# Performance work log

Hardware: AMD Instinct MI355X
Metric: run time of the kernel (lower is better)

Reference implementation:

```python
import jax, jax.numpy as jnp
import numpy as np

EPS_NORM = 1e-12  # F.normalize eps
LN_EPS = 1e-5


def _ln(x, g, b):
    mu = x.mean(-1, keepdims=True)
    var = ((x - mu) ** 2).mean(-1, keepdims=True)
    return (x - mu) / jnp.sqrt(var + LN_EPS) * g + b


def _gate(x, w1, b1, g, b, w2, b2):
    # Linear -> LayerNorm(32) -> SiLU -> Linear -> Sigmoid, squeeze(-1)
    t = _ln(x @ w1 + b1, g, b)
    t = jax.nn.silu(t)
    return jax.nn.sigmoid(t @ w2 + b2)[..., 0]


def setup_inputs() -> dict:
    key = jax.random.key(0)
    B, N, D, dH, S, HID = 4, 4096, 1024, 256, 256, 32
    ks = jax.random.split(key, 24)
    sc_d = 0.5 * (6.0 / (D + dH)) ** 0.5  # xavier gain=0.5 approx
    sc_h = 0.5 * (6.0 / (D + HID)) ** 0.5
    inp = {
        "h": jax.random.normal(ks[0], (B, N, D), jnp.float32),
        # encoder complex projection (stored as (in,out))
        "Wr": jax.random.uniform(ks[1], (D, dH), jnp.float32, -sc_d, sc_d),
        "br": jnp.zeros((dH,), jnp.float32),
        "Wi": jax.random.uniform(ks[2], (D, dH), jnp.float32, -sc_d, sc_d),
        "bi": jnp.zeros((dH,), jnp.float32),
        # uncertainty net
        "uw1": jax.random.uniform(ks[3], (D, HID), jnp.float32, -sc_h, sc_h),
        "ub1": jnp.zeros((HID,), jnp.float32),
        "ug": jnp.ones((HID,), jnp.float32),
        "ubeta": jnp.zeros((HID,), jnp.float32),
        "uw2": jax.random.uniform(ks[4], (HID, 1), jnp.float32, -0.2, 0.2),
        "ub2": jnp.zeros((1,), jnp.float32),
        # decoherence gamma net
        "gw1": jax.random.uniform(ks[5], (D, HID), jnp.float32, -sc_h, sc_h),
        "gb1": jnp.zeros((HID,), jnp.float32),
        "gg": jnp.ones((HID,), jnp.float32),
        "gbeta": jnp.zeros((HID,), jnp.float32),
        "gw2": jax.random.uniform(ks[6], (HID, 1), jnp.float32, -0.2, 0.2),
        "gb2": jnp.zeros((1,), jnp.float32),
        # memory attention params
        "m_real": jax.random.normal(ks[7], (S, dH), jnp.float32) / dH ** 0.5,
        "m_imag": jax.random.normal(ks[8], (S, dH), jnp.float32) / dH ** 0.5,
        "values": jax.random.normal(ks[9], (S, D), jnp.float32) * 0.02,
        "ow": jax.random.uniform(ks[10], (D, D), jnp.float32, -0.5 * (3.0 / D) ** 0.5, 0.5 * (3.0 / D) ** 0.5),
        "ob": jnp.zeros((D,), jnp.float32),
        # norms
        "n1g": jnp.ones((D,), jnp.float32),
        "n1b": jnp.zeros((D,), jnp.float32),
        "n2g": jnp.ones((D,), jnp.float32),
        "n2b": jnp.zeros((D,), jnp.float32),
        # FFN
        "fw1": jax.random.normal(ks[11], (D, 4 * D), jnp.float32) * (2.0 / (5 * D)) ** 0.5,
        "fb1": jnp.zeros((4 * D,), jnp.float32),
        "fw2": jax.random.normal(ks[12], (4 * D, D), jnp.float32) * (2.0 / (5 * D)) ** 0.5,
        "fb2": jnp.zeros((D,), jnp.float32),
    }
    return inp


def reference(h, Wr, br, Wi, bi,
              uw1, ub1, ug, ubeta, uw2, ub2,
              gw1, gb1, gg, gbeta, gw2, gb2,
              m_real, m_imag, values, ow, ob,
              n1g, n1b, n2g, n2b, fw1, fb1, fw2, fb2):
    dH = m_real.shape[-1]
    # --- QuantumStateEncoder: psi = normalize(complex(Wr h, Wi h)), p in [0,0.95]
    pr = h @ Wr + br                       # (B,N,dH) real part
    pi = h @ Wi + bi                       # (B,N,dH) imag part
    nrm = jnp.maximum(jnp.sqrt(jnp.sum(pr * pr + pi * pi, -1, keepdims=True)), EPS_NORM)
    pr, pi = pr / nrm, pi / nrm
    p_init = _gate(h, uw1, ub1, ug, ubeta, uw2, ub2) * 0.95   # (B,N)
    # --- ContextualDecoherenceLayer: ctx = mean over N (identical per token)
    ctx = h.mean(axis=1)                   # (B,D)
    gamma = _gate(ctx, gw1, gb1, gg, gbeta, gw2, gb2)          # (B,)
    p = p_init * (1.0 - gamma[:, None])    # (B,N)
    # --- ExternalQuantumMemoryAttention
    mnrm = jnp.maximum(jnp.sqrt(jnp.sum(m_real * m_real + m_imag * m_imag, -1, keepdims=True)), EPS_NORM)
    Mr, Mi = m_real / mnrm, m_imag / mnrm  # (S,dH)
    # <psi|m> = sum conj(psi)*m ; |.|^2 is re^2+im^2
    re = jnp.einsum('bnd,sd->bns', pr, Mr) + jnp.einsum('bnd,sd->bns', pi, Mi)
    im = jnp.einsum('bnd,sd->bns', pr, Mi) - jnp.einsum('bnd,sd->bns', pi, Mr)
    overlap = re * re + im * im            # (B,N,S)
    raw = (1.0 - p)[..., None] * overlap + (p / dH)[..., None]
    attn = raw / (raw.sum(-1, keepdims=True) + 1e-8)
    attn_out = jnp.einsum('bns,sd->bnd', attn, values) @ ow + ob
    # --- residual + LN + FFN (dropout = eval identity)
    h1 = _ln(h + attn_out, n1g, n1b)
    ff = jax.nn.gelu(h1 @ fw1 + fb1, approximate=False) @ fw2 + fb2
    return _ln(h1 + ff, n2g, n2b)
```

## Files before the change

kernel.cpp:

```cpp
#include <hip/hip_runtime.h>
#include <math.h>


#define B_ 4
#define N_ 4096
#define D_ 1024
#define DH_ 256
#define S_ 256
#define HID_ 32
#define M_ (B_ * N_)

typedef unsigned short u16;
typedef unsigned int u32;
typedef __attribute__((ext_vector_type(8))) short bfrag;
typedef __attribute__((ext_vector_type(4))) float ffrag;

__device__ __forceinline__ float b2f(u16 u) {
    return __uint_as_float(((unsigned)u) << 16);
}
__device__ __forceinline__ u16 f2b(float f) {
    unsigned u = __float_as_uint(f);
    return (u16)((u + 0x7FFFu + ((u >> 16) & 1u)) >> 16);
}
__device__ __forceinline__ float fast_erf(float x) {
    float ax = fabsf(x);
    float t = __builtin_amdgcn_rcpf(fmaf(0.3275911f, ax, 1.f));
    float p = t * fmaf(t, fmaf(t, fmaf(t, fmaf(t, 1.061405429f, -1.453152027f),
                                       1.421413741f), -0.284496736f),
                       0.254829592f);
    float e = __expf(-ax * ax);
    float y = fmaf(-p, e, 1.f);
    return copysignf(y, x);
}
__device__ __forceinline__ float gelu_fast(float x) {
    return 0.5f * x * (1.0f + fast_erf(x * 0.70710678118654752440f));
}
__device__ __forceinline__ float ldf(const void* p, size_t i, bool bf) {
    return bf ? b2f(((const u16*)p)[i]) : ((const float*)p)[i];
}
__device__ __forceinline__ bool detect_bf(const void* n1g) {
    return *(const unsigned*)n1g == 0x3F803F80u;
}
__device__ __forceinline__ void gload16(const void* g, void* lds) {
    __builtin_amdgcn_global_load_lds(
        (const __attribute__((address_space(1))) u32*)g,
        (__attribute__((address_space(3))) u32*)lds, 16, 0, 0);
}

__global__ void zero_kernel(float* __restrict__ p, int n) {
    int i = blockIdx.x * 256 + threadIdx.x;
    if (i < n) p[i] = 0.f;
}

__global__ __launch_bounds__(256)
void h2b_kernel(const void* __restrict__ h, u16* __restrict__ hB,
                const void* __restrict__ n1g) {
    const bool bf = detect_bf(n1g);
    const size_t i = ((size_t)blockIdx.x * 256 + threadIdx.x) * 8;
    if (bf) {
        *(uint4*)(hB + i) = *(const uint4*)((const u16*)h + i);
    } else {
        const float* hf = (const float*)h;
        float4 x = *(const float4*)(hf + i);
        float4 y = *(const float4*)(hf + i + 4);
        union { u16 u[8]; uint4 v; } pk;
        pk.u[0] = f2b(x.x); pk.u[1] = f2b(x.y);
        pk.u[2] = f2b(x.z); pk.u[3] = f2b(x.w);
        pk.u[4] = f2b(y.x); pk.u[5] = f2b(y.y);
        pk.u[6] = f2b(y.z); pk.u[7] = f2b(y.w);
        *(uint4*)(hB + i) = pk.v;
    }
}

__global__ void pack_bias_kernel(const void* __restrict__ br,
                                 const void* __restrict__ bi,
                                 void* __restrict__ brbi,
                                 const void* __restrict__ n1g) {
    const bool bf = detect_bf(n1g);
    const int t = threadIdx.x;
    if (bf) {
        ((u16*)brbi)[t]       = ((const u16*)br)[t];
        ((u16*)brbi)[256 + t] = ((const u16*)bi)[t];
    } else {
        ((float*)brbi)[t]       = ((const float*)br)[t];
        ((float*)brbi)[256 + t] = ((const float*)bi)[t];
    }
}

__global__ __launch_bounds__(256)
void transpose_w_kernel(const void* __restrict__ W, u16* __restrict__ WT,
                        int K, int N, const void* __restrict__ n1g) {
    const bool bf = detect_bf(n1g);
    __shared__ u16 t[64][65];
    const int n0 = blockIdx.x * 64, k0 = blockIdx.y * 64;
    const int a = threadIdx.x & 63, b = threadIdx.x >> 6;
#pragma unroll
    for (int r = 0; r < 16; ++r) {
        int k = b * 16 + r;
        t[k][a] = f2b(ldf(W, (size_t)(k0 + k) * N + n0 + a, bf));
    }
    __syncthreads();
#pragma unroll
    for (int r = 0; r < 16; ++r) {
        int n = b * 16 + r;
        WT[(size_t)(n0 + n) * K + k0 + a] = t[a][n];
    }
}

__global__ __launch_bounds__(256)
void ctx_sum_kernel(const u16* __restrict__ hB, float* __restrict__ ctx) {
    const int chunks = N_ / 128;
    const int b = blockIdx.x / chunks;
    const int ch = blockIdx.x % chunks;
    const int tid = threadIdx.x;
    const int colg = (tid & 127) * 8;
    const int rp = tid >> 7;
    const size_t base = ((size_t)b * N_ + (size_t)ch * 128) * D_;
    float a[8] = {};
    for (int r = rp; r < 128; r += 2) {
        uint4 v = *(const uint4*)(hB + base + (size_t)r * D_ + colg);
        const u16* u = (const u16*)&v;
#pragma unroll
        for (int q = 0; q < 8; ++q) a[q] += b2f(u[q]);
    }
#pragma unroll
    for (int q = 0; q < 8; ++q)
        atomicAdd(&ctx[b * D_ + colg + q], a[q]);
}

__global__ __launch_bounds__(128)
void gamma_gate_kernel(const float* __restrict__ ctx,
                       const void* __restrict__ w1, const void* __restrict__ b1,
                       const void* __restrict__ g, const void* __restrict__ beta,
                       const void* __restrict__ w2, const void* __restrict__ b2,
                       float* __restrict__ out, const void* __restrict__ n1g) {
    const bool bf = detect_bf(n1g);
    const int row = blockIdx.x;
    const int tid = threadIdx.x;
    const int col = tid & 31;
    const int chunk = tid >> 5;
    const float xscale = 1.f / (float)N_;

    float acc = 0.f;
    for (int k = chunk * 256; k < chunk * 256 + 256; ++k)
        acc += ctx[(size_t)row * D_ + k] * xscale * ldf(w1, (size_t)k * HID_ + col, bf);

    __shared__ float part[4][HID_];
    __shared__ float s[HID_];
    __shared__ float mu_s, rstd_s;
    part[chunk][col] = acc;
    __syncthreads();
    if (tid < HID_)
        s[tid] = part[0][tid] + part[1][tid] + part[2][tid] + part[3][tid]
               + ldf(b1, tid, bf);
    __syncthreads();
    if (tid == 0) {
        float m = 0.f;
        for (int i = 0; i < HID_; ++i) m += s[i];
        m /= (float)HID_;
        float var = 0.f;
        for (int i = 0; i < HID_; ++i) { float dd = s[i] - m; var += dd * dd; }
        var /= (float)HID_;
        mu_s = m;
        rstd_s = rsqrtf(var + 1e-5f);
    }
    __syncthreads();
    if (tid < HID_) {
        float v = (s[tid] - mu_s) * rstd_s * ldf(g, tid, bf) + ldf(beta, tid, bf);
        v = v / (1.f + expf(-v));
        s[tid] = v * ldf(w2, tid, bf);
    }
    __syncthreads();
    if (tid == 0) {
        float z = 0.f;
        for (int i = 0; i < HID_; ++i) z += s[i];
        z += ldf(b2, 0, bf);
        out[row] = 1.f / (1.f + expf(-z));
    }
}

__global__ __launch_bounds__(128)
void p_gate_kernel(const u16* __restrict__ hB,
                   const void* __restrict__ w1, const void* __restrict__ b1,
                   const void* __restrict__ g, const void* __restrict__ beta,
                   const void* __restrict__ w2, const void* __restrict__ b2,
                   float* __restrict__ out, const void* __restrict__ n1g) {
    const bool bf = detect_bf(n1g);
    const int row = blockIdx.x;
    const int tid = threadIdx.x;
    const int col = tid & 31;
    const int chunk = tid >> 5;

    float acc = 0.f;
    for (int k = chunk * 256; k < chunk * 256 + 256; ++k)
        acc += b2f(hB[(size_t)row * D_ + k]) * ldf(w1, (size_t)k * HID_ + col, bf);

    __shared__ float part[4][HID_];
    __shared__ float s[HID_];
    __shared__ float mu_s, rstd_s;
    part[chunk][col] = acc;
    __syncthreads();
    if (tid < HID_)
        s[tid] = part[0][tid] + part[1][tid] + part[2][tid] + part[3][tid]
               + ldf(b1, tid, bf);
    __syncthreads();
    if (tid == 0) {
        float m = 0.f;
        for (int i = 0; i < HID_; ++i) m += s[i];
        m /= (float)HID_;
        float var = 0.f;
        for (int i = 0; i < HID_; ++i) { float dd = s[i] - m; var += dd * dd; }
        var /= (float)HID_;
        mu_s = m;
        rstd_s = rsqrtf(var + 1e-5f);
    }
    __syncthreads();
    if (tid < HID_) {
        float v = (s[tid] - mu_s) * rstd_s * ldf(g, tid, bf) + ldf(beta, tid, bf);
        v = v / (1.f + expf(-v));
        s[tid] = v * ldf(w2, tid, bf);
    }
    __syncthreads();
    if (tid == 0) {
        float z = 0.f;
        for (int i = 0; i < HID_; ++i) z += s[i];
        z += ldf(b2, 0, bf);
        out[row] = 0.95f / (1.f + expf(-z));
    }
}

__global__ __launch_bounds__(256)
void norm_m_kernel(const void* __restrict__ m_real, const void* __restrict__ m_imag,
                   u16* __restrict__ bcatT, const void* __restrict__ n1g) {
    const bool bf = detect_bf(n1g);
    const int s = blockIdx.x;
    const int d = threadIdx.x;
    float mr = ldf(m_real, (size_t)s * DH_ + d, bf);
    float mi = ldf(m_imag, (size_t)s * DH_ + d, bf);
    float v = mr * mr + mi * mi;
#pragma unroll
    for (int off = 32; off; off >>= 1) v += __shfl_down(v, off, 64);
    __shared__ float red[4];
    if ((d & 63) == 0) red[d >> 6] = v;
    __syncthreads();
    float tot = red[0] + red[1] + red[2] + red[3];
    float inv = 1.f / fmaxf(sqrtf(tot), 1e-12f);
    float nr = mr * inv, ni = mi * inv;
    bcatT[(size_t)s * 512 + d]               = f2b(nr);
    bcatT[(size_t)s * 512 + 256 + d]         = f2b(ni);
    bcatT[(size_t)(256 + s) * 512 + d]       = f2b(ni);
    bcatT[(size_t)(256 + s) * 512 + 256 + d] = f2b(-nr);
}

__global__ __launch_bounds__(256)
void gemm_mfma(const u16* __restrict__ A, const u16* __restrict__ WT,
               const void* __restrict__ bias, void* __restrict__ out,
               int kseg, int lda, int ldw, int ldo,
               int act, int fo32, const void* __restrict__ n1g) {
    const bool bf = detect_bf(n1g);
    __shared__ short As[128 * 64];
    __shared__ short Bs[128 * 64];
    const int tid = threadIdx.x;

    const int nwg = gridDim.x * gridDim.y;
    const int flat = blockIdx.y * gridDim.x + blockIdx.x;
    const int xcd = flat & 7, idx = flat >> 3;
    const int qq = nwg >> 3, rr = nwg & 7;
    const int nf = (xcd < rr ? xcd * (qq + 1) : rr * (qq + 1) + (xcd - rr) * qq) + idx;
    const int c0 = (nf % gridDim.x) * 128;
    const int r0 = (nf / gridDim.x) * 128;

    const int lane = tid & 63, wave = tid >> 6;
    const int wm = wave & 1, wn = wave >> 1;
    const int quad = lane >> 4, l15 = lane & 15;
    const int l8 = lane >> 3;
    const int lc = (lane & 7) ^ l8;
    const int sx = l15 & 7;

    ffrag acc[4][4];
#pragma unroll
    for (int i = 0; i < 4; ++i)
#pragma unroll
        for (int j = 0; j < 4; ++j)
            acc[i][j] = (ffrag){0.f, 0.f, 0.f, 0.f};

    for (int k0 = 0; k0 < kseg; k0 += 64) {
        __syncthreads();
#pragma unroll
        for (int i = 0; i < 4; ++i) {
            int rb = wave * 32 + i * 8;
            gload16(A + (size_t)(r0 + rb + l8) * lda + k0 + lc * 8, &As[rb * 64]);
        }
#pragma unroll
        for (int i = 0; i < 4; ++i) {
            int rb = wave * 32 + i * 8;
            gload16(WT + (size_t)(c0 + rb + l8) * ldw + k0 + lc * 8, &Bs[rb * 64]);
        }
        __syncthreads();

#pragma unroll
        for (int ks = 0; ks < 2; ++ks) {
            bfrag a[4], b[4];
#pragma unroll
            for (int i = 0; i < 4; ++i) {
                int row = wm * 64 + i * 16 + l15;
                a[i] = *(const bfrag*)&As[row * 64 + (((ks * 4 + quad) ^ sx) * 8)];
            }
#pragma unroll
            for (int j = 0; j < 4; ++j) {
                int row = wn * 64 + j * 16 + l15;
                b[j] = *(const bfrag*)&Bs[row * 64 + (((ks * 4 + quad) ^ sx) * 8)];
            }
#pragma unroll
            for (int i = 0; i < 4; ++i)
#pragma unroll
                for (int j = 0; j < 4; ++j)
                    acc[i][j] = __builtin_amdgcn_mfma_f32_16x16x32_bf16(
                        a[i], b[j], acc[i][j], 0, 0, 0);
        }
    }

    float bv[4];
#pragma unroll
    for (int j = 0; j < 4; ++j)
        bv[j] = bias ? ldf(bias, c0 + wn * 64 + j * 16 + l15, bf) : 0.f;
#pragma unroll
    for (int i = 0; i < 4; ++i)
#pragma unroll
        for (int r = 0; r < 4; ++r) {
            int row_g = r0 + wm * 64 + i * 16 + quad * 4 + r;
#pragma unroll
            for (int j = 0; j < 4; ++j) {
                int col_g = c0 + wn * 64 + j * 16 + l15;
                float v = acc[i][j][r] + bv[j];
                if (act) v = gelu_fast(v);
                if (fo32) ((float*)out)[(size_t)row_g * ldo + col_g] = v;
                else      ((u16*)out)[(size_t)row_g * ldo + col_g] = f2b(v);
            }
        }
}

__global__ __launch_bounds__(512, 2)
void gemm_mfma2(const u16* __restrict__ A, const u16* __restrict__ WT,
                const void* __restrict__ bias, void* __restrict__ out,
                int K, int lda, int ldw, int ldo,
                int act, int fo32, const void* __restrict__ n1g) {
    const bool bf = detect_bf(n1g);
    __shared__ short As[2][256 * 64];
    __shared__ short Bs[2][256 * 64];
    const int tid = threadIdx.x;

    const int nwg = gridDim.x * gridDim.y;
    const int flat = blockIdx.y * gridDim.x + blockIdx.x;
    const int xcd = flat & 7, idx = flat >> 3;
    const int qq = nwg >> 3, rr = nwg & 7;
    const int nf = (xcd < rr ? xcd * (qq + 1) : rr * (qq + 1) + (xcd - rr) * qq) + idx;
    const int c0 = (nf % gridDim.x) * 256;
    const int r0 = (nf / gridDim.x) * 256;

    const int lane = tid & 63, wave = tid >> 6;
    const int wm = wave & 1, wn = wave >> 1;
    const int quad = lane >> 4, l15 = lane & 15;
    const int l8 = lane >> 3;
    const int lc = (lane & 7) ^ l8;
    const int sx = l15 & 7;

    ffrag acc[8][4];
#pragma unroll
    for (int i = 0; i < 8; ++i)
#pragma unroll
        for (int j = 0; j < 4; ++j)
            acc[i][j] = (ffrag){0.f, 0.f, 0.f, 0.f};

    auto STAGE_PIECE = [&](int buf, int k0, int pc) {
        int rb = pc * 64 + wave * 8;
        gload16(A + (size_t)(r0 + rb + l8) * lda + k0 + lc * 8,
                &As[buf][rb * 64]);
        gload16(WT + (size_t)(c0 + rb + l8) * ldw + k0 + lc * 8,
                &Bs[buf][rb * 64]);
    };

    bfrag a[8], b[4];
    auto PHASE_DS = [&](int buf, int ks) {
#pragma unroll
        for (int j = 0; j < 4; ++j) {
            int row = wn * 64 + j * 16 + l15;
            b[j] = *(const bfrag*)&Bs[buf][row * 64 + (((ks * 4 + quad) ^ sx) * 8)];
        }
#pragma unroll
        for (int i = 0; i < 8; ++i) {
            int row = wm * 128 + i * 16 + l15;
            a[i] = *(const bfrag*)&As[buf][row * 64 + (((ks * 4 + quad) ^ sx) * 8)];
        }
    };
    auto PHASE_MFMA = [&]() {
#pragma unroll
        for (int i = 0; i < 8; ++i)
#pragma unroll
            for (int j = 0; j < 4; ++j)
                acc[i][j] = __builtin_amdgcn_mfma_f32_16x16x32_bf16(
                    a[i], b[j], acc[i][j], 0, 0, 0);
    };

    const int nt = K >> 6;
#pragma unroll
    for (int pc = 0; pc < 4; ++pc) STAGE_PIECE(0, 0, pc);
    int cur = 0;
    for (int t = 0; t < nt; ++t) {
        const int kn = (t + 1) << 6;
        const bool pre = (t + 1 < nt);
        if (pre) {
            STAGE_PIECE(cur ^ 1, kn, 0);
            STAGE_PIECE(cur ^ 1, kn, 1);
            asm volatile("s_waitcnt vmcnt(4)" ::: "memory");
        } else {
            asm volatile("s_waitcnt vmcnt(0)" ::: "memory");
        }
        __builtin_amdgcn_s_barrier();
        PHASE_DS(cur, 0);
        asm volatile("s_waitcnt lgkmcnt(0)" ::: "memory");
        __builtin_amdgcn_sched_barrier(0);
        __builtin_amdgcn_s_setprio(1);
        PHASE_MFMA();
        __builtin_amdgcn_s_setprio(0);
        __builtin_amdgcn_sched_barrier(0);
        PHASE_DS(cur, 1);
        if (pre) {
            STAGE_PIECE(cur ^ 1, kn, 2);
            STAGE_PIECE(cur ^ 1, kn, 3);
        }
        __builtin_amdgcn_s_barrier();
        asm volatile("s_waitcnt lgkmcnt(0)" ::: "memory");
        __builtin_amdgcn_sched_barrier(0);
        __builtin_amdgcn_s_setprio(1);
        PHASE_MFMA();
        __builtin_amdgcn_s_setprio(0);
        __builtin_amdgcn_sched_barrier(0);
        __builtin_amdgcn_s_barrier();
        cur ^= 1;
    }

    float bv[4];
#pragma unroll
    for (int j = 0; j < 4; ++j)
        bv[j] = bias ? ldf(bias, c0 + wn * 64 + j * 16 + l15, bf) : 0.f;
#pragma unroll
    for (int i = 0; i < 8; ++i)
#pragma unroll
        for (int r = 0; r < 4; ++r) {
            int row_g = r0 + wm * 128 + i * 16 + quad * 4 + r;
#pragma unroll
            for (int j = 0; j < 4; ++j) {
                int col_g = c0 + wn * 64 + j * 16 + l15;
                float v = acc[i][j][r] + bv[j];
                if (act) v = gelu_fast(v);
                if (fo32) ((float*)out)[(size_t)row_g * ldo + col_g] = v;
                else      ((u16*)out)[(size_t)row_g * ldo + col_g] = f2b(v);
            }
        }
}

#define TPW 8
__global__ __launch_bounds__(256)
void attn_weights_kernel(const u16* __restrict__ psi,
                         const float* __restrict__ reim,
                         const float* __restrict__ p_init,
                         const float* __restrict__ gamma,
                         u16* __restrict__ a2) {
    const int token0 = blockIdx.x * TPW;
    const int tid = threadIdx.x;
    __shared__ float red[4];

    for (int tt = 0; tt < TPW; ++tt) {
        const size_t t = (size_t)(token0 + tt);
        float x0 = b2f(psi[t * 512 + tid]);
        float x1 = b2f(psi[t * 512 + 256 + tid]);
        float v = x0 * x0 + x1 * x1;
#pragma unroll
        for (int off = 32; off; off >>= 1) v += __shfl_down(v, off, 64);
        if ((tid & 63) == 0) red[tid >> 6] = v;
        __syncthreads();
        float inv = 1.f / fmaxf(red[0] + red[1] + red[2] + red[3], 1e-24f);

        float p = p_init[t] * (1.f - gamma[t / N_]);
        float re = reim[t * 512 + tid];
        float im = reim[t * 512 + 256 + tid];
        float raw = (1.f - p) * (re * re + im * im) * inv + p * (1.f / (float)DH_);

        float w = raw;
#pragma unroll
        for (int off = 32; off; off >>= 1) w += __shfl_down(w, off, 64);
        __syncthreads();
        if ((tid & 63) == 0) red[tid >> 6] = w;
        __syncthreads();
        float denom = red[0] + red[1] + red[2] + red[3];
        a2[t * 256 + tid] = f2b(raw / (denom + 1e-8f));
        __syncthreads();
    }
}

__global__ __launch_bounds__(256)
void copy_rows_kernel(const u16* __restrict__ src, u16* __restrict__ dst) {
    const int row = blockIdx.x;
    const int tid = threadIdx.x;
#pragma unroll
    for (int q = 0; q < 4; ++q)
        dst[(size_t)row * D_ + q * 256 + tid] = src[(size_t)row * D_ + q * 256 + tid];
}

__global__ __launch_bounds__(256)
void ln_add_kernel(const void* __restrict__ x, int xmode, size_t xrow0,
                   const void* __restrict__ y, int ymode,
                   const void* __restrict__ g, const void* __restrict__ b,
                   u16* __restrict__ outB, float* __restrict__ outF,
                   const void* __restrict__ n1g) {
    const bool bfin = detect_bf(n1g);
    const bool bfx = (xmode == 1) ? true : bfin;
    const int row = blockIdx.x;
    const int tid = threadIdx.x;
    __shared__ float red[4];

    float v[4];
#pragma unroll
    for (int q = 0; q < 4; ++q) {
        int d = q * 256 + tid;
        float yv = ymode ? ((const float*)y)[(size_t)row * D_ + d]
                         : b2f(((const u16*)y)[(size_t)row * D_ + d]);
        v[q] = ldf(x, (xrow0 + row) * (size_t)D_ + d, bfx) + yv;
    }

    float s = v[0] + v[1] + v[2] + v[3];
#pragma unroll
    for (int off = 32; off; off >>= 1) s += __shfl_down(s, off, 64);
    if ((tid & 63) == 0) red[tid >> 6] = s;
    __syncthreads();
    float mu = (red[0] + red[1] + red[2] + red[3]) * (1.f / (float)D_);
    __syncthreads();

    float q2 = 0.f;
#pragma unroll
    for (int j = 0; j < 4; ++j) { float dd = v[j] - mu; q2 += dd * dd; }
#pragma unroll
    for (int off = 32; off; off >>= 1) q2 += __shfl_down(q2, off, 64);
    if ((tid & 63) == 0) red[tid >> 6] = q2;
    __syncthreads();
    float var = (red[0] + red[1] + red[2] + red[3]) * (1.f / (float)D_);
    float rstd = rsqrtf(var + 1e-5f);

#pragma unroll
    for (int q = 0; q < 4; ++q) {
        int d = q * 256 + tid;
        float o = (v[q] - mu) * rstd * ldf(g, d, bfin) + ldf(b, d, bfin);
        if (outF) outF[(size_t)row * D_ + d] = o;
        else      outB[(size_t)row * D_ + d] = f2b(o);
    }
}

extern "C" void kernel_launch(void* const* d_in, const int* in_sizes, int n_in,
                              void* d_out, int out_size, void* d_ws, size_t ws_size,
                              hipStream_t stream) {
    const void* h      = d_in[0];
    const void* Wr     = d_in[1];
    const void* br     = d_in[2];
    const void* Wi     = d_in[3];
    const void* bi     = d_in[4];
    const void* uw1    = d_in[5];
    const void* ub1    = d_in[6];
    const void* ug     = d_in[7];
    const void* ubeta  = d_in[8];
    const void* uw2    = d_in[9];
    const void* ub2    = d_in[10];
    const void* gw1    = d_in[11];
    const void* gb1    = d_in[12];
    const void* gg     = d_in[13];
    const void* gbeta  = d_in[14];
    const void* gw2    = d_in[15];
    const void* gb2    = d_in[16];
    const void* m_real = d_in[17];
    const void* m_imag = d_in[18];
    const void* values = d_in[19];
    const void* ow     = d_in[20];
    const void* ob     = d_in[21];
    const void* n1g    = d_in[22];
    const void* n1b    = d_in[23];
    const void* n2g    = d_in[24];
    const void* n2b    = d_in[25];
    const void* fw1    = d_in[26];
    const void* fb1    = d_in[27];
    const void* fw2    = d_in[28];
    const void* fb2    = d_in[29];

    char*  ws      = (char*)d_ws;
    float* ctx     = (float*)(ws);
    float* gammap  = (float*)(ws + 16384);
    float* p_init  = (float*)(ws + 16448);
    void*  brbi    = (void*)(ws + 81984);
    u16*   BCatT   = (u16*)(ws + 84032);
    u16*   WrT     = (u16*)(ws + 608320);
    u16*   WiT     = (u16*)(ws + 1132608);
    u16*   owT     = (u16*)(ws + 2181184);
    u16*   fw1T    = (u16*)(ws + 4278336);
    u16*   fw2T    = (u16*)(ws + 12666944);
    const size_t tbase = 21055552;

    int CH = 16384;
    while (CH > 256 && tbase + (size_t)CH * 12288 > ws_size) CH >>= 1;
    u16*   t_buf = (u16*)(ws + tbase);
    float* pf    = (float*)(t_buf + (size_t)CH * 4096);

    float* outF    = (float*)d_out;
    u16*   Psi     = (u16*)d_out;
    u16*   A2      = Psi + (size_t)M_ * 512;
    u16*   VOT     = A2 + (size_t)M_ * 256;
    u16*   valuesB = VOT + (size_t)D_ * S_;
    u16*   X2      = (u16*)d_out + (size_t)M_ * D_;
    u16*   hB      = X2;
    float* REIMf   = (float*)X2;

    h2b_kernel<<<M_ * D_ / 2048, 256, 0, stream>>>(h, hB, n1g);
    h2b_kernel<<<S_ * D_ / 2048, 256, 0, stream>>>(values, valuesB, n1g);

    transpose_w_kernel<<<dim3(DH_ / 64, D_ / 64), 256, 0, stream>>>(Wr, WrT, D_, DH_, n1g);
    transpose_w_kernel<<<dim3(DH_ / 64, D_ / 64), 256, 0, stream>>>(Wi, WiT, D_, DH_, n1g);
    transpose_w_kernel<<<dim3(D_ / 64, D_ / 64), 256, 0, stream>>>(ow, owT, D_, D_, n1g);
    transpose_w_kernel<<<dim3(4 * D_ / 64, D_ / 64), 256, 0, stream>>>(fw1, fw1T, D_, 4 * D_, n1g);
    transpose_w_kernel<<<dim3(D_ / 64, 4 * D_ / 64), 256, 0, stream>>>(fw2, fw2T, 4 * D_, D_, n1g);
    pack_bias_kernel<<<1, 256, 0, stream>>>(br, bi, brbi, n1g);

    gemm_mfma<<<dim3(S_ / 128, D_ / 128), 256, 0, stream>>>(
        owT, valuesB, nullptr, VOT, D_, D_, D_, S_, 0, 0, n1g);

    zero_kernel<<<16, 256, 0, stream>>>(ctx, B_ * D_);
    ctx_sum_kernel<<<B_ * (N_ / 128), 256, 0, stream>>>(hB, ctx);
    gamma_gate_kernel<<<B_, 128, 0, stream>>>(ctx, gw1, gb1, gg, gbeta,
                                              gw2, gb2, gammap, n1g);

    norm_m_kernel<<<S_, 256, 0, stream>>>(m_real, m_imag, BCatT, n1g);

    gemm_mfma<<<dim3(512 / 128, M_ / 128), 256, 0, stream>>>(
        hB, WrT, brbi, Psi, D_, D_, D_, 512, 0, 0, n1g);

    p_gate_kernel<<<M_, 128, 0, stream>>>(hB, uw1, ub1, ug, ubeta,
                                          uw2, ub2, p_init, n1g);

    gemm_mfma<<<dim3(512 / 128, M_ / 128), 256, 0, stream>>>(
        Psi, BCatT, nullptr, REIMf, 512, 512, 512, 512, 0, 1, n1g);

    attn_weights_kernel<<<M_ / TPW, 256, 0, stream>>>(Psi, REIMf, p_init,
                                                      gammap, A2);

    for (int c = 0; c < M_ / CH; ++c) {
        const size_t offh = (size_t)c * CH * D_;
        gemm_mfma2<<<dim3(D_ / 256, CH / 256), 512, 0, stream>>>(
            A2 + (size_t)c * CH * S_, VOT, ob, pf, S_, S_, S_, D_, 0, 1, n1g);
        ln_add_kernel<<<CH, 256, 0, stream>>>(h, 0, (size_t)c * CH, pf, 1,
                                              n1g, n1b, X2 + offh, nullptr, n1g);
    }

    for (int c = 0; c < M_ / CH; ++c) {
        const size_t off = (size_t)c * CH * D_;
        gemm_mfma2<<<dim3(4 * D_ / 256, CH / 256), 512, 0, stream>>>(
            X2 + off, fw1T, fb1, t_buf, D_, D_, D_, 4 * D_, 1, 0, n1g);
        gemm_mfma2<<<dim3(D_ / 256, CH / 256), 512, 0, stream>>>(
            t_buf, fw2T, fb2, pf, 4 * D_, 4 * D_, 4 * D_, D_, 0, 1, n1g);
        copy_rows_kernel<<<CH, 256, 0, stream>>>(X2 + off, t_buf);
        ln_add_kernel<<<CH, 256, 0, stream>>>(t_buf, 1, 0, pf, 1,
                                              n2g, n2b, nullptr, outF + off, n1g);
    }
}
```

Baseline: 969.1 us.

## Single-buffer LDS in 256x256 GEMM to double occupancy per CU

Replaces the double-buffered shared-memory tiles in gemm_mfma2 with a single buffer, halving LDS use to 64KB, and raises the launch-bounds occupancy hint from 2 to 4 blocks. Loads for the next K tile now start only after the current tile's MFMA work and a barrier finish. The intent is to hide global-load latency through more resident workgroups instead of in-block prefetch. The risk is that with 512 threads and a 32-fragment accumulator per thread, register pressure may prevent the higher occupancy, leaving load latency exposed.

Measured after the change: 3.618 ms. 273% more time.

```diff
diff --git a/kernel.cpp b/kernel.cpp
--- a/kernel.cpp
+++ b/kernel.cpp
@@ -340,14 +340,14 @@
         }
 }
 
-__global__ __launch_bounds__(512, 2)
+__global__ __launch_bounds__(512, 4)
 void gemm_mfma2(const u16* __restrict__ A, const u16* __restrict__ WT,
                 const void* __restrict__ bias, void* __restrict__ out,
                 int K, int lda, int ldw, int ldo,
                 int act, int fo32, const void* __restrict__ n1g) {
     const bool bf = detect_bf(n1g);
-    __shared__ short As[2][256 * 64];
-    __shared__ short Bs[2][256 * 64];
+    __shared__ short As[256 * 64];
+    __shared__ short Bs[256 * 64];
     const int tid = threadIdx.x;
 
     const int nwg = gridDim.x * gridDim.y;
@@ -372,25 +372,25 @@
         for (int j = 0; j < 4; ++j)
             acc[i][j] = (ffrag){0.f, 0.f, 0.f, 0.f};
 
-    auto STAGE_PIECE = [&](int buf, int k0, int pc) {
+    auto STAGE_PIECE = [&](int k0, int pc) {
         int rb = pc * 64 + wave * 8;
         gload16(A + (size_t)(r0 + rb + l8) * lda + k0 + lc * 8,
-                &As[buf][rb * 64]);
+                &As[rb * 64]);
         gload16(WT + (size_t)(c0 + rb + l8) * ldw + k0 + lc * 8,
-                &Bs[buf][rb * 64]);
+                &Bs[rb * 64]);
     };
 
     bfrag a[8], b[4];
-    auto PHASE_DS = [&](int buf, int ks) {
+    auto PHASE_DS = [&](int ks) {
 #pragma unroll
         for (int j = 0; j < 4; ++j) {
             int row = wn * 64 + j * 16 + l15;
-            b[j] = *(const bfrag*)&Bs[buf][row * 64 + (((ks * 4 + quad) ^ sx) * 8)];
+            b[j] = *(const bfrag*)&Bs[row * 64 + (((ks * 4 + quad) ^ sx) * 8)];
         }
 #pragma unroll
         for (int i = 0; i < 8; ++i) {
             int row = wm * 128 + i * 16 + l15;
-            a[i] = *(const bfrag*)&As[buf][row * 64 + (((ks * 4 + quad) ^ sx) * 8)];
+            a[i] = *(const bfrag*)&As[row * 64 + (((ks * 4 + quad) ^ sx) * 8)];
         }
     };
     auto PHASE_MFMA = [&]() {
@@ -404,32 +404,18 @@
 
     const int nt = K >> 6;
 #pragma unroll
-    for (int pc = 0; pc < 4; ++pc) STAGE_PIECE(0, 0, pc);
-    int cur = 0;
+    for (int pc = 0; pc < 4; ++pc) STAGE_PIECE(0, pc);
     for (int t = 0; t < nt; ++t) {
-        const int kn = (t + 1) << 6;
-        const bool pre = (t + 1 < nt);
-        if (pre) {
-            STAGE_PIECE(cur ^ 1, kn, 0);
-            STAGE_PIECE(cur ^ 1, kn, 1);
-            asm volatile("s_waitcnt vmcnt(4)" ::: "memory");
-        } else {
-            asm volatile("s_waitcnt vmcnt(0)" ::: "memory");
-        }
+        asm volatile("s_waitcnt vmcnt(0)" ::: "memory");
         __builtin_amdgcn_s_barrier();
-        PHASE_DS(cur, 0);
+        PHASE_DS(0);
         asm volatile("s_waitcnt lgkmcnt(0)" ::: "memory");
         __builtin_amdgcn_sched_barrier(0);
         __builtin_amdgcn_s_setprio(1);
         PHASE_MFMA();
         __builtin_amdgcn_s_setprio(0);
         __builtin_amdgcn_sched_barrier(0);
-        PHASE_DS(cur, 1);
-        if (pre) {
-            STAGE_PIECE(cur ^ 1, kn, 2);
-            STAGE_PIECE(cur ^ 1, kn, 3);
-        }
-        __builtin_amdgcn_s_barrier();
+        PHASE_DS(1);
         asm volatile("s_waitcnt lgkmcnt(0)" ::: "memory");
         __builtin_amdgcn_sched_barrier(0);
         __builtin_amdgcn_s_setprio(1);
@@ -437,7 +423,11 @@
         __builtin_amdgcn_s_setprio(0);
         __builtin_amdgcn_sched_barrier(0);
         __builtin_amdgcn_s_barrier();
-        cur ^= 1;
+        if (t + 1 < nt) {
+            const int kn = (t + 1) << 6;
+#pragma unroll
+            for (int pc = 0; pc < 4; ++pc) STAGE_PIECE(kn, pc);
+        }
     }
 
     float bv[4];
```
